# Kernel optimization log

Measured on AMD Instinct MI355X. Metric: run time of the kernel, lower is better.

Reference implementation:

```python
import jax, jax.numpy as jnp
import numpy as np

# dims: d=1024 model width, h=16 heads, d_head=64
B, S, D, H = 4, 1024, 1024, 16
RD = float(np.sqrt(D))
VAR_W_INIT = 0.001  # var_init[0]: initial weight-variance value


def setup_inputs() -> dict:
    key = jax.random.key(0)
    ks = jax.random.split(key, 5)
    x = jax.random.normal(ks[0], (B, S, D), jnp.float32)
    # input variance must be non-negative; small positive values
    var_x = jax.random.uniform(ks[1], (B, S, D), jnp.float32) * 0.01
    scale = 1.0 / np.sqrt(D)
    Wq = jax.random.normal(ks[2], (D, D), jnp.float32) * scale
    Wk = jax.random.normal(ks[3], (D, D), jnp.float32) * scale
    Wv = jax.random.normal(ks[4], (D, D), jnp.float32) * scale
    var_Wq = jnp.full((D, D), VAR_W_INIT, jnp.float32)
    var_Wk = jnp.full((D, D), VAR_W_INIT, jnp.float32)
    var_Wv = jnp.full((D, D), VAR_W_INIT, jnp.float32)
    return dict(x=x, var_x=var_x, Wq=Wq, var_Wq=var_Wq, Wk=Wk, var_Wk=var_Wk, Wv=Wv, var_Wv=var_Wv)


def _linear_vmp(x, var_x, W, var_W):
    # mean: x W^T ; variance of product of independent Gaussians:
    # var = var_x (W^2)^T + x^2 var_W^T + var_x var_W^T
    m = x @ W.T
    v = var_x @ (W * W).T + (x * x) @ var_W.T + var_x @ var_W.T
    return m, v


def _quadratic_vmp(m1, v1, m2, v2):
    # matmul of two independent Gaussian tensors (moment propagation)
    m = m1 @ m2
    v = v1 @ v2 + v1 @ (m2 * m2) + (m1 * m1) @ v2
    return m, v


def _softmax_vmp(a, var_a):
    # delta-method through softmax: J_ij = s_i(delta_ij - s_j)
    # var_i = s_i^2 [ (1-2 s_i) var_i + sum_j s_j^2 var_j ]
    s = jax.nn.softmax(a, axis=-1)
    sv = jnp.sum(s * s * var_a, axis=-1, keepdims=True)
    var_s = s * s * ((1.0 - 2.0 * s) * var_a + sv)
    return s, var_s


def _split_heads(t):
    b, s, _ = t.shape
    return t.reshape(b, s, H, D // H).transpose(0, 2, 1, 3)  # [B,H,S,dh]


def reference(x, var_x, Wq, var_Wq, Wk, var_Wk, Wv, var_Wv):
    q, vq = _linear_vmp(x, var_x, Wq, var_Wq)
    k, vk = _linear_vmp(x, var_x, Wk, var_Wk)
    v, vv = _linear_vmp(x, var_x, Wv, var_Wv)
    q, vq, k, vk, v, vv = map(_split_heads, (q, vq, k, vk, v, vv))
    kt = k.transpose(0, 1, 3, 2)
    vkt = vk.transpose(0, 1, 3, 2)
    a, va = _quadratic_vmp(q, vq, kt, vkt)          # [B,H,S,S]
    a, va = a / RD, va / (RD * RD)
    a, va = _softmax_vmp(a, va)                      # masking=False path
    o, vo = _quadratic_vmp(a, va, v, vv)             # [B,H,S,dh]
    o = o.transpose(0, 2, 1, 3).reshape(x.shape)
    vo = vo.transpose(0, 2, 1, 3).reshape(x.shape)
    # residual_vmp, mode='identity': mean add, variances add
    return x + o, var_x + vo
```

## Files before the change

### kernel.cpp

```cpp
#include <hip/hip_runtime.h>
#include <hip/hip_bf16.h>

#define BB 4
#define SS 1024
#define DD 1024
#define HH 16
#define DH 64
#define MM (BB*SS)

typedef __attribute__((ext_vector_type(8))) short bf16x8;
typedef __attribute__((ext_vector_type(8))) unsigned short u16x8;
typedef __attribute__((ext_vector_type(4))) float f32x4;

__device__ __forceinline__ float b2f(unsigned short u) {
    union { unsigned int i; float f; } c; c.i = ((unsigned int)u) << 16; return c.f;
}
__device__ __forceinline__ unsigned short f2b(float f) {
    __hip_bfloat16 h = __float2bfloat16(f);
    return *reinterpret_cast<unsigned short*>(&h);
}
__device__ __forceinline__ unsigned int pack2(float a, float b) {
    return (unsigned int)f2b(a) | ((unsigned int)f2b(b) << 16);
}
__device__ __forceinline__ void gload16(const unsigned short* g, unsigned short* l) {
    __builtin_amdgcn_global_load_lds(
        (const __attribute__((address_space(1))) void*)g,
        (__attribute__((address_space(3))) void*)l,
        16, 0, 0);
}
#define MFMA16(a, b, c) __builtin_amdgcn_mfma_f32_16x16x32_bf16(a, b, c, 0, 0, 0)

__global__ __launch_bounds__(256) void prep_x_kernel(
    const float* __restrict__ x, const float* __restrict__ vx,
    unsigned short* __restrict__ xb, unsigned short* __restrict__ vxb,
    unsigned short* __restrict__ xsb)
{
    const size_t i = ((size_t)blockIdx.x * 256 + threadIdx.x) * 4;
    float4 a = *(const float4*)(x + i);
    float4 b = *(const float4*)(vx + i);
    ushort4 oa = { f2b(a.x), f2b(a.y), f2b(a.z), f2b(a.w) };
    ushort4 ob = { f2b(b.x), f2b(b.y), f2b(b.z), f2b(b.w) };
    ushort4 os = { f2b(a.x*a.x), f2b(a.y*a.y), f2b(a.z*a.z), f2b(a.w*a.w) };
    *(ushort4*)(xb  + i) = oa;
    *(ushort4*)(vxb + i) = ob;
    *(ushort4*)(xsb + i) = os;
}

__global__ __launch_bounds__(256) void prep_w_kernel(
    const float* __restrict__ W0, const float* __restrict__ vW0,
    const float* __restrict__ W1, const float* __restrict__ vW1,
    const float* __restrict__ W2, const float* __restrict__ vW2,
    unsigned short* __restrict__ wp)
{
    const int z = blockIdx.y;
    const float* W  = (z==0)? W0 : (z==1)? W1 : W2;
    const float* vW = (z==0)? vW0: (z==1)? vW1: vW2;
    const size_t NW = (size_t)DD*DD;
    unsigned short* wb = wp + (size_t)(3*z+0)*NW;
    unsigned short* wc = wp + (size_t)(3*z+1)*NW;
    unsigned short* wv = wp + (size_t)(3*z+2)*NW;

    const size_t i = ((size_t)blockIdx.x * 256 + threadIdx.x) * 4;
    float4 a = *(const float4*)(W + i);
    float4 b = *(const float4*)(vW + i);
    ushort4 oa = { f2b(a.x), f2b(a.y), f2b(a.z), f2b(a.w) };
    ushort4 oc = { f2b(a.x*a.x + b.x), f2b(a.y*a.y + b.y),
                   f2b(a.z*a.z + b.z), f2b(a.w*a.w + b.w) };
    ushort4 ov = { f2b(b.x), f2b(b.y), f2b(b.z), f2b(b.w) };
    *(ushort4*)(wb + i) = oa;
    *(ushort4*)(wc + i) = oc;
    *(ushort4*)(wv + i) = ov;
}

__global__ __launch_bounds__(256) void gemm_proj_kernel(
    const unsigned short* __restrict__ xb, const unsigned short* __restrict__ vxb,
    const unsigned short* __restrict__ xsb,
    const unsigned short* __restrict__ wp,
    unsigned short* __restrict__ qm, unsigned short* __restrict__ km,
    unsigned short* __restrict__ vm,
    unsigned short* __restrict__ qv, unsigned short* __restrict__ kv,
    unsigned short* __restrict__ vvv)
{
    __shared__ unsigned short sA[2][128*32];
    __shared__ unsigned short sB[2][128*32];

    const int z = blockIdx.z;
    const size_t NW = (size_t)DD*DD;
    const bool isVar = (z >= 3);
    const int p = isVar ? (z - 3) : z;
    const unsigned short* A0 = isVar ? vxb : xb;
    const unsigned short* A1 = isVar ? xsb : xb;
    const unsigned short* B0 = wp + (size_t)(3*p + (isVar ? 1 : 0)) * NW;
    const unsigned short* B1 = isVar ? (wp + (size_t)(3*p + 2) * NW) : B0;
    unsigned short* Out = (z==0)? qm : (z==1)? km : (z==2)? vm
                        : (z==3)? qv : (z==4)? kv : vvv;
    const int NT = isVar ? 64 : 32;

    const int bn = blockIdx.x;
    const int bm = blockIdx.y;
    const int tid = threadIdx.x;
    const int w = tid >> 6;
    const int l = tid & 63;
    const int wr = w >> 1, wc = w & 1;

    const int r0 = tid >> 2;
    const int s0 = (((tid & 3) ^ ((r0 >> 1) & 3)) * 8);
    const size_t aoff0 = (size_t)(bm*128 + r0) * DD + s0;
    const size_t boff0 = (size_t)(bn*128 + r0) * DD + s0;
    const int ldsd0 = (w*64) * 8;
    const int ldsd1 = (256 + w*64) * 8;

#define STG(buf, t) do {                                                   \
        const unsigned short* As_ = ((t) < 32) ? A0 : A1;                  \
        const unsigned short* Bs_ = ((t) < 32) ? B0 : B1;                  \
        const int kc_ = ((t) & 31) * 32;                                   \
        gload16(As_ + aoff0 + kc_,                   &sA[buf][ldsd0]);     \
        gload16(As_ + aoff0 + (size_t)64*DD + kc_,   &sA[buf][ldsd1]);     \
        gload16(Bs_ + boff0 + kc_,                   &sB[buf][ldsd0]);     \
        gload16(Bs_ + boff0 + (size_t)64*DD + kc_,   &sB[buf][ldsd1]);     \
    } while (0)

    f32x4 acc[4][4];
    #pragma unroll
    for (int i = 0; i < 4; ++i)
        #pragma unroll
        for (int j = 0; j < 4; ++j)
            acc[i][j] = (f32x4){0.f,0.f,0.f,0.f};

    const int fr = l & 15;
    const int hi = l >> 4;

    STG(0, 0);
    __syncthreads();

    for (int t = 0; t < NT; ++t) {
        const int cb = t & 1;
        if (t + 1 < NT) STG(cb ^ 1, t + 1);

        bf16x8 bfr[4];
        #pragma unroll
        for (int j = 0; j < 4; ++j) {
            const int row = wc*64 + j*16 + fr;
            bfr[j] = *(const bf16x8*)&sB[cb][row*32 + ((hi ^ ((row >> 1) & 3)) * 8)];
        }
        #pragma unroll
        for (int i = 0; i < 4; ++i) {
            const int row = wr*64 + i*16 + fr;
            bf16x8 a0 = *(const bf16x8*)&sA[cb][row*32 + ((hi ^ ((row >> 1) & 3)) * 8)];
            #pragma unroll
            for (int j = 0; j < 4; ++j)
                acc[i][j] = MFMA16(a0, bfr[j], acc[i][j]);
        }
        __syncthreads();
    }
#undef STG

    const int orow = bm*128 + wr*64 + (hi << 2);
    const int ocol = bn*128 + wc*64 + fr;
    #pragma unroll
    for (int i = 0; i < 4; ++i)
        #pragma unroll
        for (int j = 0; j < 4; ++j)
            #pragma unroll
            for (int r = 0; r < 4; ++r)
                Out[(size_t)(orow + i*16 + r) * DD + ocol + j*16] = f2b(acc[i][j][r]);
}

__global__ __launch_bounds__(256) void prep_vt_kernel(
    const unsigned short* __restrict__ vm, const unsigned short* __restrict__ vvv,
    unsigned short* __restrict__ vt, unsigned short* __restrict__ wt,
    unsigned short* __restrict__ vvt)
{
    __shared__ unsigned short tv[64][68];
    __shared__ unsigned short tw[64][68];
    __shared__ unsigned short tvv[64][68];
    const int t = threadIdx.x;
    const int jt = blockIdx.x, h = blockIdx.y, b = blockIdx.z;
    const size_t ibase = (size_t)b*SS*DD + (size_t)h*DH;
    {
        const int j = t & 63, cg = t >> 6;
        const size_t ga = ibase + (size_t)(jt*64 + j)*DD + cg*16;
        #pragma unroll
        for (int hh = 0; hh < 2; ++hh) {
            u16x8 v8  = *(const u16x8*)(vm  + ga + hh*8);
            u16x8 vv8 = *(const u16x8*)(vvv + ga + hh*8);
            u16x8 w8;
            #pragma unroll
            for (int e = 0; e < 8; ++e) {
                float vf = b2f(v8[e]);
                w8[e] = f2b(b2f(vv8[e]) + vf*vf);
            }
            *(u16x8*)&tv[j][cg*16 + hh*8]  = v8;
            *(u16x8*)&tvv[j][cg*16 + hh*8] = vv8;
            *(u16x8*)&tw[j][cg*16 + hh*8]  = w8;
        }
    }
    __syncthreads();
    {
        const int d  = t >> 2;
        const int pc = t & 3;
        const int lc = pc ^ ((d >> 1) & 3);
        #pragma unroll
        for (int st = 0; st < 2; ++st) {
            u16x8 o0, o1, o2;
            #pragma unroll
            for (int e = 0; e < 8; ++e) {
                const int jl = st*32 + (e >> 2)*16 + lc*4 + (e & 3);
                o0[e] = tv[jl][d];
                o1[e] = tw[jl][d];
                o2[e] = tvv[jl][d];
            }
            const size_t ob = (size_t)((b*HH + h)*DH + d)*SS + jt*64 + st*32 + pc*8;
            *(u16x8*)(vt  + ob) = o0;
            *(u16x8*)(wt  + ob) = o1;
            *(u16x8*)(vvt + ob) = o2;
        }
    }
}

__global__ __launch_bounds__(256) void prep_kk_kernel(
    const unsigned short* __restrict__ kmp, const unsigned short* __restrict__ kvp,
    unsigned short* __restrict__ kkb)
{
    const size_t i = ((size_t)blockIdx.x * 256 + threadIdx.x) * 8;
    u16x8 k8 = *(const u16x8*)(kmp + i);
    u16x8 v8 = *(const u16x8*)(kvp + i);
    u16x8 o8;
    #pragma unroll
    for (int e = 0; e < 8; ++e) {
        float kf = b2f(k8[e]);
        o8[e] = f2b(b2f(v8[e]) + kf*kf);
    }
    *(u16x8*)(kkb + i) = o8;
}

union PW { unsigned int u[4]; bf16x8 v; };

__global__ __launch_bounds__(256, 3) void attn_mfma_kernel(
    const unsigned short* __restrict__ kmg, const unsigned short* __restrict__ kvg,
    const unsigned short* __restrict__ kkg,
    const unsigned short* __restrict__ vtg, const unsigned short* __restrict__ wtg,
    const unsigned short* __restrict__ vvtg,
    const unsigned short* __restrict__ qmg, const unsigned short* __restrict__ qvg,
    const float* __restrict__ x, const float* __restrict__ vx,
    float* __restrict__ om, float* __restrict__ ov)
{
    __shared__ unsigned short Ks[2][3][32*64];
    __shared__ unsigned short Vs[2][3][64*32];

    const int tid = threadIdx.x;
    const int w = tid >> 6, l = tid & 63;
    const int lo = l & 15, hi = l >> 4;

    const int fb = blockIdx.x;
    const int g  = ((fb >> 7) << 3) | (fb & 7);
    const int qt = (fb >> 3) & 15;
    const int h  = g & 15;
    const int b  = g >> 4;

    const size_t xbase = (size_t)b*SS*DD + (size_t)h*DH;
    const size_t vbase = (size_t)(b*HH + h)*DH*SS;

    bf16x8 qA[2], vqA[2], qsA[2];
    {
        const int qrow = qt*64 + w*16 + lo;
        #pragma unroll
        for (int ks = 0; ks < 2; ++ks) {
            const size_t ga = xbase + (size_t)qrow*DD + ks*32 + hi*8;
            qA[ks]  = *(const bf16x8*)(qmg + ga);
            vqA[ks] = *(const bf16x8*)(qvg + ga);
            #pragma unroll
            for (int e = 0; e < 8; ++e) {
                float f = b2f((unsigned short)qA[ks][e]);
                qsA[ks][e] = (short)f2b(f*f);
            }
        }
    }
    bf16x8 onesB;
    #pragma unroll
    for (int e = 0; e < 8; ++e) onesB[e] = (short)0x3F80;

    f32x4 T1[4], T2[4], T3[4], T4[4], T5[4];
    f32x4 zac = {0.f,0.f,0.f,0.f}, e2vac = {0.f,0.f,0.f,0.f};
    #pragma unroll
    for (int cb = 0; cb < 4; ++cb) {
        T1[cb] = (f32x4){0.f,0.f,0.f,0.f};
        T2[cb] = (f32x4){0.f,0.f,0.f,0.f};
        T3[cb] = (f32x4){0.f,0.f,0.f,0.f};
        T4[cb] = (f32x4){0.f,0.f,0.f,0.f};
        T5[cb] = (f32x4){0.f,0.f,0.f,0.f};
    }

    const size_t koff = (size_t)(l >> 3)*DD + (size_t)(((l & 7) ^ ((l >> 3) & 7)) * 8);
    const size_t voff = (size_t)(l >> 2)*SS + (size_t)((l & 3) * 8);

    const float INV_RD  = 0.03125f;
    const float INV_RD2 = 0.0009765625f;

#define IK(bu, m, p, G) gload16(G + xbase + (j0 + (size_t)(p)*8)*DD + koff, &Ks[bu][m][(p)*512])
#define IV(bu, m, p, G) gload16(G + vbase + (size_t)((p)*16)*SS + j0 + voff, &Vs[bu][m][(p)*512])
#define STAGE(tt, bu) do {                                                     \
        const size_t j0 = (size_t)(tt) * 32;                                   \
        if (w == 0)      { IK(bu,0,0,kmg); IK(bu,0,1,kmg); IK(bu,0,2,kmg);     \
                           IK(bu,0,3,kmg); IK(bu,1,0,kvg); IK(bu,1,1,kvg); }   \
        else if (w == 1) { IK(bu,1,2,kvg); IK(bu,1,3,kvg); IK(bu,2,0,kkg);     \
                           IK(bu,2,1,kkg); IK(bu,2,2,kkg); IK(bu,2,3,kkg); }   \
        else if (w == 2) { IV(bu,0,0,vtg); IV(bu,0,1,vtg); IV(bu,0,2,vtg);     \
                           IV(bu,0,3,vtg); IV(bu,1,0,wtg); IV(bu,1,1,wtg); }   \
        else             { IV(bu,1,2,wtg); IV(bu,1,3,wtg); IV(bu,2,0,vvtg);    \
                           IV(bu,2,1,vvtg); IV(bu,2,2,vvtg); IV(bu,2,3,vvtg); }\
    } while (0)

    STAGE(0, 0);
    __syncthreads();

    int cur = 0;
    for (int t = 0; t < SS/32; ++t) {
        if (t + 1 < SS/32) STAGE(t + 1, cur ^ 1);

        PW pe, pe2, pev, pe3;
        #pragma unroll
        for (int jb = 0; jb < 2; ++jb) {
            f32x4 aa = {0.f,0.f,0.f,0.f}, vva = {0.f,0.f,0.f,0.f};
            const int jrow = jb*16 + lo;
            #pragma unroll
            for (int ks = 0; ks < 2; ++ks) {
                const int co = jrow*64 + (((ks*4 + hi) ^ (lo & 7)) * 8);
                bf16x8 kB  = *(const bf16x8*)&Ks[cur][0][co];
                bf16x8 vkB = *(const bf16x8*)&Ks[cur][1][co];
                bf16x8 kkB = *(const bf16x8*)&Ks[cur][2][co];
                aa  = MFMA16(kB,  qA[ks],  aa);
                vva = MFMA16(kkB, vqA[ks], vva);
                vva = MFMA16(vkB, qsA[ks], vva);
            }
            #pragma unroll
            for (int rp = 0; rp < 2; ++rp) {
                float a0 = aa[rp*2]   * INV_RD,  va0 = vva[rp*2]   * INV_RD2;
                float a1 = aa[rp*2+1] * INV_RD,  va1 = vva[rp*2+1] * INV_RD2;
                float e0 = __expf(a0), e1 = __expf(a1);
                float s0 = e0*e0,      s1 = e1*e1;
                float v0 = s0*va0,     v1 = s1*va1;
                float t0 = v0*e0,      t1 = v1*e1;
                pe.u [jb*2+rp] = pack2(e0, e1);
                pe2.u[jb*2+rp] = pack2(s0, s1);
                pev.u[jb*2+rp] = pack2(v0, v1);
                pe3.u[jb*2+rp] = pack2(t0, t1);
            }
        }

        zac   = MFMA16(pe.v,  onesB, zac);
        e2vac = MFMA16(pev.v, onesB, e2vac);
        #pragma unroll
        for (int cb = 0; cb < 4; ++cb) {
            const int vo = (cb*16 + lo)*32 + ((hi ^ ((lo >> 1) & 3)) * 8);
            bf16x8 vB  = *(const bf16x8*)&Vs[cur][0][vo];
            bf16x8 wB  = *(const bf16x8*)&Vs[cur][1][vo];
            bf16x8 vvB = *(const bf16x8*)&Vs[cur][2][vo];
            T1[cb] = MFMA16(pe.v,  vB,  T1[cb]);
            T2[cb] = MFMA16(pev.v, wB,  T2[cb]);
            T3[cb] = MFMA16(pe3.v, wB,  T3[cb]);
            T4[cb] = MFMA16(pe2.v, wB,  T4[cb]);
            T5[cb] = MFMA16(pe2.v, vvB, T5[cb]);
        }

        __syncthreads();
        cur ^= 1;
    }

    #pragma unroll
    for (int r = 0; r < 4; ++r) {
        const float Z     = zac[r];
        const float invZ  = 1.f / Z;
        const float invZ2 = invZ * invZ;
        const float sv    = e2vac[r] * invZ2;
        const int row = qt*64 + w*16 + hi*4 + r;
        #pragma unroll
        for (int cb = 0; cb < 4; ++cb) {
            const size_t gi = xbase + (size_t)row*DD + cb*16 + lo;
            const float o  = T1[cb][r] * invZ;
            const float vo = (T2[cb][r] + sv*T4[cb][r] + T5[cb][r]) * invZ2
                           - 2.f * T3[cb][r] * invZ2 * invZ;
            om[gi] = x[gi] + o;
            ov[gi] = vx[gi] + vo;
        }
    }
#undef IK
#undef IV
#undef STAGE
}

extern "C" void kernel_launch(void* const* d_in, const int* in_sizes, int n_in,
                              void* d_out, int out_size, void* d_ws, size_t ws_size,
                              hipStream_t stream) {
    const float* x    = (const float*)d_in[0];
    const float* vx   = (const float*)d_in[1];
    const float* Wq   = (const float*)d_in[2];
    const float* vWq  = (const float*)d_in[3];
    const float* Wk   = (const float*)d_in[4];
    const float* vWk  = (const float*)d_in[5];
    const float* Wv   = (const float*)d_in[6];
    const float* vWv  = (const float*)d_in[7];

    const size_t NE = (size_t)MM * DD;
    const size_t NW = (size_t)DD * DD;

    unsigned short* u = (unsigned short*)d_ws;
    unsigned short* qm   = u + 0*NE;
    unsigned short* qv   = u + 1*NE;
    unsigned short* km   = u + 2*NE;
    unsigned short* kv   = u + 3*NE;
    unsigned short* vm   = u + 4*NE;
    unsigned short* vvv  = u + 5*NE;
    unsigned short* xbb  = u + 6*NE;
    unsigned short* vxbb = u + 7*NE;
    unsigned short* xsbb = u + 8*NE;
    unsigned short* wp   = u + 9*NE;

    float* om = (float*)d_out;
    float* ov = om + NE;

    prep_x_kernel<<<4096, 256, 0, stream>>>(x, vx, xbb, vxbb, xsbb);
    prep_w_kernel<<<dim3(1024, 3), 256, 0, stream>>>(Wq, vWq, Wk, vWk, Wv, vWv, wp);

    dim3 gg(8, 32, 6);
    gemm_proj_kernel<<<gg, 256, 0, stream>>>(xbb, vxbb, xsbb, wp,
                                             qm, km, vm, qv, kv, vvv);

    unsigned short* vt  = xbb;
    unsigned short* wt  = vxbb;
    unsigned short* vvt = xsbb;
    unsigned short* kkb = wp;
    dim3 gt(SS/64, HH, BB);
    prep_vt_kernel<<<gt, 256, 0, stream>>>(vm, vvv, vt, wt, vvt);
    prep_kk_kernel<<<2048, 256, 0, stream>>>(km, kv, kkb);

    attn_mfma_kernel<<<1024, 256, 0, stream>>>(km, kv, kkb, vt, wt, vvt,
                                               qm, qv, x, vx, om, ov);
}
```

Measured before the change: 204.6 us.

## Use 512-thread attention blocks covering 128 query rows, sharing K/V tiles

The attention kernel now launches 512 blocks of 512 threads, so each block handles 128 query rows with eight waves. Each staged K/V tile is reused by twice as many rows, and the global-to-LDS copy work is split across eight waves. The exponent now uses exp2f with a prescaled constant, and the variance scaling by 1/D is moved from the inner loop to the epilogue. MFMA sections are wrapped in s_setprio to favour matrix issue. Risks are higher register pressure under the 512,2 launch bounds, fewer blocks to fill the CUs, and costlier block-wide barriers.

```diff
diff --git a/kernel.cpp b/kernel.cpp
--- a/kernel.cpp
+++ b/kernel.cpp
@@ -236,7 +236,7 @@
 
 union PW { unsigned int u[4]; bf16x8 v; };
 
-__global__ __launch_bounds__(256, 3) void attn_mfma_kernel(
+__global__ __launch_bounds__(512, 2) void attn_mfma_kernel(
     const unsigned short* __restrict__ kmg, const unsigned short* __restrict__ kvg,
     const unsigned short* __restrict__ kkg,
     const unsigned short* __restrict__ vtg, const unsigned short* __restrict__ wtg,
@@ -253,8 +253,8 @@
     const int lo = l & 15, hi = l >> 4;
 
     const int fb = blockIdx.x;
-    const int g  = ((fb >> 7) << 3) | (fb & 7);
-    const int qt = (fb >> 3) & 15;
+    const int qt = (fb >> 3) & 7;
+    const int g  = ((fb >> 6) << 3) | (fb & 7);
     const int h  = g & 15;
     const int b  = g >> 4;
 
@@ -263,7 +263,7 @@
 
     bf16x8 qA[2], vqA[2], qsA[2];
     {
-        const int qrow = qt*64 + w*16 + lo;
+        const int qrow = qt*128 + w*16 + lo;
         #pragma unroll
         for (int ks = 0; ks < 2; ++ks) {
             const size_t ga = xbase + (size_t)qrow*DD + ks*32 + hi*8;
@@ -294,21 +294,22 @@
     const size_t koff = (size_t)(l >> 3)*DD + (size_t)(((l & 7) ^ ((l >> 3) & 7)) * 8);
     const size_t voff = (size_t)(l >> 2)*SS + (size_t)((l & 3) * 8);
 
-    const float INV_RD  = 0.03125f;
-    const float INV_RD2 = 0.0009765625f;
+    const float KE = 0.03125f * 1.44269504f;
 
 #define IK(bu, m, p, G) gload16(G + xbase + (j0 + (size_t)(p)*8)*DD + koff, &Ks[bu][m][(p)*512])
 #define IV(bu, m, p, G) gload16(G + vbase + (size_t)((p)*16)*SS + j0 + voff, &Vs[bu][m][(p)*512])
-#define STAGE(tt, bu) do {                                                     \
-        const size_t j0 = (size_t)(tt) * 32;                                   \
-        if (w == 0)      { IK(bu,0,0,kmg); IK(bu,0,1,kmg); IK(bu,0,2,kmg);     \
-                           IK(bu,0,3,kmg); IK(bu,1,0,kvg); IK(bu,1,1,kvg); }   \
-        else if (w == 1) { IK(bu,1,2,kvg); IK(bu,1,3,kvg); IK(bu,2,0,kkg);     \
-                           IK(bu,2,1,kkg); IK(bu,2,2,kkg); IK(bu,2,3,kkg); }   \
-        else if (w == 2) { IV(bu,0,0,vtg); IV(bu,0,1,vtg); IV(bu,0,2,vtg);     \
-                           IV(bu,0,3,vtg); IV(bu,1,0,wtg); IV(bu,1,1,wtg); }   \
-        else             { IV(bu,1,2,wtg); IV(bu,1,3,wtg); IV(bu,2,0,vvtg);    \
-                           IV(bu,2,1,vvtg); IV(bu,2,2,vvtg); IV(bu,2,3,vvtg); }\
+#define STAGE(tt, bu) do {                                                       \
+        const size_t j0 = (size_t)(tt) * 32;                                     \
+        switch (w) {                                                             \
+        case 0:  IK(bu,0,0,kmg); IK(bu,0,1,kmg); IK(bu,0,2,kmg);  break;         \
+        case 1:  IK(bu,0,3,kmg); IK(bu,1,0,kvg); IK(bu,1,1,kvg);  break;         \
+        case 2:  IK(bu,1,2,kvg); IK(bu,1,3,kvg); IK(bu,2,0,kkg);  break;         \
+        case 3:  IK(bu,2,1,kkg); IK(bu,2,2,kkg); IK(bu,2,3,kkg);  break;         \
+        case 4:  IV(bu,0,0,vtg); IV(bu,0,1,vtg); IV(bu,0,2,vtg);  break;         \
+        case 5:  IV(bu,0,3,vtg); IV(bu,1,0,wtg); IV(bu,1,1,wtg);  break;         \
+        case 6:  IV(bu,1,2,wtg); IV(bu,1,3,wtg); IV(bu,2,0,vvtg); break;         \
+        default: IV(bu,2,1,vvtg); IV(bu,2,2,vvtg); IV(bu,2,3,vvtg); break;       \
+        }                                                                        \
     } while (0)
 
     STAGE(0, 0);
@@ -335,12 +336,12 @@
             }
             #pragma unroll
             for (int rp = 0; rp < 2; ++rp) {
-                float a0 = aa[rp*2]   * INV_RD,  va0 = vva[rp*2]   * INV_RD2;
-                float a1 = aa[rp*2+1] * INV_RD,  va1 = vva[rp*2+1] * INV_RD2;
-                float e0 = __expf(a0), e1 = __expf(a1);
-                float s0 = e0*e0,      s1 = e1*e1;
-                float v0 = s0*va0,     v1 = s1*va1;
-                float t0 = v0*e0,      t1 = v1*e1;
+                float e0 = exp2f(aa[rp*2]   * KE);
+                float e1 = exp2f(aa[rp*2+1] * KE);
+                float va0 = vva[rp*2], va1 = vva[rp*2+1];
+                float s0 = e0*e0,  s1 = e1*e1;
+                float v0 = s0*va0, v1 = s1*va1;
+                float t0 = v0*e0,  t1 = v1*e1;
                 pe.u [jb*2+rp] = pack2(e0, e1);
                 pe2.u[jb*2+rp] = pack2(s0, s1);
                 pev.u[jb*2+rp] = pack2(v0, v1);
@@ -348,6 +349,7 @@
             }
         }
 
+        __builtin_amdgcn_s_setprio(1);
         zac   = MFMA16(pe.v,  onesB, zac);
         e2vac = MFMA16(pev.v, onesB, e2vac);
         #pragma unroll
@@ -362,24 +364,26 @@
             T4[cb] = MFMA16(pe2.v, wB,  T4[cb]);
             T5[cb] = MFMA16(pe2.v, vvB, T5[cb]);
         }
+        __builtin_amdgcn_s_setprio(0);
 
         __syncthreads();
         cur ^= 1;
     }
 
+    const float IRD2 = 0.0009765625f;
     #pragma unroll
     for (int r = 0; r < 4; ++r) {
         const float Z     = zac[r];
         const float invZ  = 1.f / Z;
         const float invZ2 = invZ * invZ;
-        const float sv    = e2vac[r] * invZ2;
-        const int row = qt*64 + w*16 + hi*4 + r;
+        const float sv    = e2vac[r] * IRD2 * invZ2;
+        const int row = qt*128 + w*16 + hi*4 + r;
         #pragma unroll
         for (int cb = 0; cb < 4; ++cb) {
             const size_t gi = xbase + (size_t)row*DD + cb*16 + lo;
             const float o  = T1[cb][r] * invZ;
-            const float vo = (T2[cb][r] + sv*T4[cb][r] + T5[cb][r]) * invZ2
-                           - 2.f * T3[cb][r] * invZ2 * invZ;
+            const float vo = (T2[cb][r]*IRD2 + sv*T4[cb][r] + T5[cb][r]) * invZ2
+                           - 2.f * T3[cb][r] * IRD2 * invZ2 * invZ;
             om[gi] = x[gi] + o;
             ov[gi] = vx[gi] + vo;
         }
@@ -434,6 +438,6 @@
     prep_vt_kernel<<<gt, 256, 0, stream>>>(vm, vvv, vt, wt, vvt);
     prep_kk_kernel<<<2048, 256, 0, stream>>>(km, kv, kkb);
 
-    attn_mfma_kernel<<<1024, 256, 0, stream>>>(km, kv, kkb, vt, wt, vvt,
-                                               qm, qv, x, vx, om, ov);
-}
+    attn_mfma_kernel<<<512, 512, 0, stream>>>(km, kv, kkb, vt, wt, vvt,
+                                              qm, qv, x, vx, om, ov);
+}
```

After: 215.8 us. 5.4% more time.
